# Kernel tuning notes

Measured on AMD Instinct MI355X. Metric: run time of the kernel, lower is better.

Reference implementation:

```python
import jax, jax.numpy as jnp
import numpy as np

B, T, C = 1, 4096, 1024
H = 16
D = C // H  # head_dim = 64


def setup_inputs() -> dict:
    key = jax.random.key(0)
    ks = jax.random.split(key, 9)
    s = 1.0 / np.sqrt(C)
    return {
        "x": jax.random.normal(ks[0], (B, T, C), dtype=jnp.float32),
        "Wq": jax.random.normal(ks[1], (C, C), dtype=jnp.float32) * s,
        "bq": jnp.zeros((C,), dtype=jnp.float32),
        "Wk": jax.random.normal(ks[2], (C, C), dtype=jnp.float32) * s,
        "bk": jnp.zeros((C,), dtype=jnp.float32),
        "Wv": jax.random.normal(ks[3], (C, C), dtype=jnp.float32) * s,
        "bv": jnp.zeros((C,), dtype=jnp.float32),
        "Wo": jax.random.normal(ks[4], (C, C), dtype=jnp.float32) * s,
        "bo": jnp.zeros((C,), dtype=jnp.float32),
    }


def reference(x, Wq, bq, Wk, bk, Wv, bv, Wo, bo):
    # QKV projections (torch Linear: y = x @ W.T + b)
    q = x @ Wq.T + bq
    k = x @ Wk.T + bk
    v = x @ Wv.T + bv
    # [B,T,C] -> [B,H,T,D]
    q = q.reshape(B, T, H, D).transpose(0, 2, 1, 3)
    k = k.reshape(B, T, H, D).transpose(0, 2, 1, 3)
    v = v.reshape(B, T, H, D).transpose(0, 2, 1, 3)
    scale = 1.0 / jnp.sqrt(jnp.asarray(D, dtype=q.dtype))
    scores = jnp.einsum("bhqd,bhkd->bhqk", q, k) * scale  # [B,H,T,T]
    attn = jax.nn.softmax(scores, axis=-1)
    out = jnp.einsum("bhqk,bhkd->bhqd", attn, v)  # [B,H,T,D]
    out = out.transpose(0, 2, 1, 3).reshape(B, T, C)
    return out @ Wo.T + bo
```

## Files before the change

### kernel.cpp

```cpp
#include <hip/hip_runtime.h>
#include <stdint.h>

#define T_SEQ 4096
#define CDIM  1024
#define NH    16
#define DH    64

typedef _Float16 half8 __attribute__((ext_vector_type(8)));
typedef _Float16 half4 __attribute__((ext_vector_type(4)));
typedef float    f32x4 __attribute__((ext_vector_type(4)));

#if __has_builtin(__builtin_amdgcn_exp2f)
#define EXP2F(x) __builtin_amdgcn_exp2f(x)
#else
#define EXP2F(x) exp2f(x)
#endif

#define MFMA_K32(a, b, c) __builtin_amdgcn_mfma_f32_16x16x32_f16(a, b, c, 0, 0, 0)
#define MFMA_K16(a, b, c) __builtin_amdgcn_mfma_f32_16x16x16f16(a, b, c, 0, 0, 0)

__device__ __forceinline__ void gl_lds16(const void* g, void* l) {
  __builtin_amdgcn_global_load_lds(
      (const __attribute__((address_space(1))) uint32_t*)g,
      (__attribute__((address_space(3))) uint32_t*)l, 16, 0, 0);
}

__global__ void cvt_kernel(const float* __restrict__ src, _Float16* __restrict__ dst, int n) {
  int i = (blockIdx.x * blockDim.x + threadIdx.x) * 8;
  if (i >= n) return;
  float4 f0 = *(const float4*)(src + i);
  float4 f1 = *(const float4*)(src + i + 4);
  half8 h = { (_Float16)f0.x, (_Float16)f0.y, (_Float16)f0.z, (_Float16)f0.w,
              (_Float16)f1.x, (_Float16)f1.y, (_Float16)f1.z, (_Float16)f1.w };
  *(half8*)(dst + i) = h;
}

__global__ void cvt_w4_kernel(const float* __restrict__ w0, const float* __restrict__ w1,
                              const float* __restrict__ w2, const float* __restrict__ w3,
                              _Float16* __restrict__ o0, _Float16* __restrict__ o1,
                              _Float16* __restrict__ o2, _Float16* __restrict__ o3) {
  const float* src = (blockIdx.y == 0) ? w0 : (blockIdx.y == 1) ? w1 : (blockIdx.y == 2) ? w2 : w3;
  _Float16*    dst = (blockIdx.y == 0) ? o0 : (blockIdx.y == 1) ? o1 : (blockIdx.y == 2) ? o2 : o3;
  int i = (blockIdx.x * blockDim.x + threadIdx.x) * 8;
  float4 f0 = *(const float4*)(src + i);
  float4 f1 = *(const float4*)(src + i + 4);
  half8 h = { (_Float16)f0.x, (_Float16)f0.y, (_Float16)f0.z, (_Float16)f0.w,
              (_Float16)f1.x, (_Float16)f1.y, (_Float16)f1.z, (_Float16)f1.w };
  *(half8*)(dst + i) = h;
}

__device__ __forceinline__ void gemm_core(const _Float16* __restrict__ A,
                                          const _Float16* __restrict__ Bm,
                                          _Float16* As, _Float16* Bs,
                                          int bm, int bn,
                                          f32x4 (&acc)[4][4]) {
  const int tid  = threadIdx.x;
  const int lane = tid & 63;
  const int wave = tid >> 6;
  const int waveM = wave >> 1, waveN = wave & 1;
  const int quad = lane >> 4, c16 = lane & 15;

  const int rs0 = wave * 32 + (lane >> 2);
  const int rs1 = rs0 + 16;
  const int dm0 = ((lane & 3) ^ ((rs0 >> 1) & 3)) * 8;
  const int dm1 = ((lane & 3) ^ ((rs1 >> 1) & 3)) * 8;

  const _Float16* gA0 = A  + (size_t)(bm * 128 + rs0) * CDIM + dm0;
  const _Float16* gA1 = A  + (size_t)(bm * 128 + rs1) * CDIM + dm1;
  const _Float16* gB0 = Bm + (size_t)(bn * 128 + rs0) * CDIM + dm0;
  const _Float16* gB1 = Bm + (size_t)(bn * 128 + rs1) * CDIM + dm1;
  _Float16* lA0 = As + wave * 1024;
  _Float16* lA1 = lA0 + 512;
  _Float16* lB0 = Bs + wave * 1024;
  _Float16* lB1 = lB0 + 512;

  const int xsw  = (c16 >> 1) & 3;
  const int offA = (waveM * 64 + c16) * 32 + ((quad ^ xsw) * 8);
  const int offB = (waveN * 64 + c16) * 32 + ((quad ^ xsw) * 8);

  for (int kk = 0; kk < 32; ++kk) {
    gl_lds16(gA0, lA0);
    gl_lds16(gA1, lA1);
    gl_lds16(gB0, lB0);
    gl_lds16(gB1, lB1);
    __syncthreads();
    half8 a[4], b[4];
#pragma unroll
    for (int i = 0; i < 4; ++i) a[i] = *(const half8*)(As + offA + i * 512);
#pragma unroll
    for (int i = 0; i < 4; ++i) b[i] = *(const half8*)(Bs + offB + i * 512);
#pragma unroll
    for (int mi = 0; mi < 4; ++mi)
#pragma unroll
      for (int ni = 0; ni < 4; ++ni)
        acc[mi][ni] = MFMA_K32(a[mi], b[ni], acc[mi][ni]);
    gA0 += 32; gA1 += 32; gB0 += 32; gB1 += 32;
    __syncthreads();
  }
}

__device__ __forceinline__ void gemm_core64(const _Float16* __restrict__ A,
                                            const _Float16* __restrict__ Bm,
                                            _Float16* As, _Float16* Bs,
                                            int bm, int bn,
                                            f32x4 (&acc)[2][4]) {
  const int tid  = threadIdx.x;
  const int lane = tid & 63;
  const int wave = tid >> 6;
  const int waveM = wave >> 1, waveN = wave & 1;
  const int quad = lane >> 4, c16 = lane & 15;

  const int rsA = wave * 16 + (lane >> 2);
  const int dmA = ((lane & 3) ^ ((rsA >> 1) & 3)) * 8;
  const int rs0 = wave * 32 + (lane >> 2);
  const int rs1 = rs0 + 16;
  const int dm0 = ((lane & 3) ^ ((rs0 >> 1) & 3)) * 8;
  const int dm1 = ((lane & 3) ^ ((rs1 >> 1) & 3)) * 8;

  const _Float16* gA0 = A  + (size_t)(bm * 64  + rsA) * CDIM + dmA;
  const _Float16* gB0 = Bm + (size_t)(bn * 128 + rs0) * CDIM + dm0;
  const _Float16* gB1 = Bm + (size_t)(bn * 128 + rs1) * CDIM + dm1;
  _Float16* lA0 = As + wave * 512;
  _Float16* lB0 = Bs + wave * 1024;
  _Float16* lB1 = lB0 + 512;

  const int xsw  = (c16 >> 1) & 3;
  const int offA = (waveM * 32 + c16) * 32 + ((quad ^ xsw) * 8);
  const int offB = (waveN * 64 + c16) * 32 + ((quad ^ xsw) * 8);

  for (int kk = 0; kk < 32; ++kk) {
    gl_lds16(gA0, lA0);
    gl_lds16(gB0, lB0);
    gl_lds16(gB1, lB1);
    __syncthreads();
    half8 a[2], b[4];
#pragma unroll
    for (int i = 0; i < 2; ++i) a[i] = *(const half8*)(As + offA + i * 512);
#pragma unroll
    for (int i = 0; i < 4; ++i) b[i] = *(const half8*)(Bs + offB + i * 512);
#pragma unroll
    for (int mi = 0; mi < 2; ++mi)
#pragma unroll
      for (int ni = 0; ni < 4; ++ni)
        acc[mi][ni] = MFMA_K32(a[mi], b[ni], acc[mi][ni]);
    gA0 += 32; gB0 += 32; gB1 += 32;
    __syncthreads();
  }
}

__global__ __launch_bounds__(256) void qkv_gemm(
    const _Float16* __restrict__ xh,
    const _Float16* __restrict__ wqh, const _Float16* __restrict__ wkh, const _Float16* __restrict__ wvh,
    const float* __restrict__ bq, const float* __restrict__ bk, const float* __restrict__ bv,
    _Float16* __restrict__ qh, _Float16* __restrict__ kh, _Float16* __restrict__ vth) {
  __shared__ __align__(16) _Float16 As[128 * 32];
  __shared__ __align__(16) _Float16 Bs[128 * 32];
  const int z = blockIdx.z;
  const _Float16* W   = (z == 0) ? wqh : ((z == 1) ? wkh : wvh);
  const float*    bias = (z == 0) ? bq  : ((z == 1) ? bk  : bv);

  f32x4 acc[4][4];
  const f32x4 zf = {0.f, 0.f, 0.f, 0.f};
#pragma unroll
  for (int i = 0; i < 4; ++i)
#pragma unroll
    for (int j = 0; j < 4; ++j) acc[i][j] = zf;

  gemm_core(xh, W, As, Bs, blockIdx.x, blockIdx.y, acc);

  const int lane = threadIdx.x & 63, wave = threadIdx.x >> 6;
  const int waveM = wave >> 1, waveN = wave & 1;
  const int quad = lane >> 4, c16 = lane & 15;
  const int rowb = blockIdx.x * 128 + waveM * 64;
  const int colb = blockIdx.y * 128 + waveN * 64;

  float bsv[4];
#pragma unroll
  for (int ni = 0; ni < 4; ++ni) bsv[ni] = bias[colb + ni * 16 + c16];

  if (z < 2) {
    _Float16* outp = (z == 0) ? qh : kh;
    const float scl = (z == 0) ? 0.18033688011112042f : 1.0f;
#pragma unroll
    for (int mi = 0; mi < 4; ++mi)
#pragma unroll
      for (int ni = 0; ni < 4; ++ni) {
        int col = colb + ni * 16 + c16;
        int hh = col >> 6, dd = col & 63;
#pragma unroll
        for (int r = 0; r < 4; ++r) {
          int row = rowb + mi * 16 + quad * 4 + r;
          outp[(size_t)(hh * T_SEQ + row) * DH + dd] = (_Float16)((acc[mi][ni][r] + bsv[ni]) * scl);
        }
      }
  } else {
#pragma unroll
    for (int mi = 0; mi < 4; ++mi)
#pragma unroll
      for (int ni = 0; ni < 4; ++ni) {
        int col  = colb + ni * 16 + c16;
        int row0 = rowb + mi * 16 + quad * 4;
        half4 h4;
#pragma unroll
        for (int r = 0; r < 4; ++r) h4[r] = (_Float16)(acc[mi][ni][r] + bsv[ni]);
        *(half4*)(vth + (size_t)col * T_SEQ + row0) = h4;
      }
  }
}

__global__ __launch_bounds__(256) void out_gemm(
    const _Float16* __restrict__ ctx, const _Float16* __restrict__ woh,
    const float* __restrict__ bo, float* __restrict__ out) {
  __shared__ __align__(16) _Float16 As[64 * 32];
  __shared__ __align__(16) _Float16 Bs[128 * 32];
  f32x4 acc[2][4];
  const f32x4 zf = {0.f, 0.f, 0.f, 0.f};
#pragma unroll
  for (int i = 0; i < 2; ++i)
#pragma unroll
    for (int j = 0; j < 4; ++j) acc[i][j] = zf;

  gemm_core64(ctx, woh, As, Bs, blockIdx.x, blockIdx.y, acc);

  const int lane = threadIdx.x & 63, wave = threadIdx.x >> 6;
  const int waveM = wave >> 1, waveN = wave & 1;
  const int quad = lane >> 4, c16 = lane & 15;
  const int rowb = blockIdx.x * 64 + waveM * 32;
  const int colb = blockIdx.y * 128 + waveN * 64;

  float bsv[4];
#pragma unroll
  for (int ni = 0; ni < 4; ++ni) bsv[ni] = bo[colb + ni * 16 + c16];

#pragma unroll
  for (int mi = 0; mi < 2; ++mi)
#pragma unroll
    for (int ni = 0; ni < 4; ++ni) {
      int col = colb + ni * 16 + c16;
#pragma unroll
      for (int r = 0; r < 4; ++r) {
        int row = rowb + mi * 16 + quad * 4 + r;
        out[(size_t)row * CDIM + col] = acc[mi][ni][r] + bsv[ni];
      }
    }
}

__global__ __launch_bounds__(256) void attn_kernel(
    const _Float16* __restrict__ qh, const _Float16* __restrict__ kh,
    const _Float16* __restrict__ vth, _Float16* __restrict__ ctx) {
  __shared__ __align__(16) _Float16 KV[2][2][64 * 64];

  const int tid = threadIdx.x, lane = tid & 63, wave = tid >> 6;
  const int quad = lane >> 4, c16 = lane & 15;
  const int h = blockIdx.y;
  const int qw = blockIdx.x * 128 + wave * 32;

  half8 qf[2][2];
#pragma unroll
  for (int qg = 0; qg < 2; ++qg)
#pragma unroll
    for (int c = 0; c < 2; ++c)
      qf[qg][c] = *(const half8*)(qh + (size_t)(h * T_SEQ + qw + qg * 16 + c16) * DH + c * 32 + quad * 8);

  const int rs0 = wave * 16 + (lane >> 3);
  const int rs1 = rs0 + 8;
  const int dm0 = ((lane & 7) ^ (rs0 & 7)) * 8;
  const int dm1 = ((lane & 7) ^ (rs1 & 7)) * 8;
  const _Float16* gK0 = kh  + (size_t)(h * T_SEQ + rs0) * DH + dm0;
  const _Float16* gK1 = kh  + (size_t)(h * T_SEQ + rs1) * DH + dm1;
  const _Float16* gV0 = vth + (size_t)(h * DH + rs0) * T_SEQ + dm0;
  const _Float16* gV1 = vth + (size_t)(h * DH + rs1) * T_SEQ + dm1;
  const int lo0 = wave * 1024, lo1 = wave * 1024 + 512;

  f32x4 o[2][4];
  f32x4 lacc[2];
  const f32x4 zf = {0.f, 0.f, 0.f, 0.f};
#pragma unroll
  for (int qg = 0; qg < 2; ++qg) {
#pragma unroll
    for (int db = 0; db < 4; ++db) o[qg][db] = zf;
    lacc[qg] = zf;
  }
  const half4 ones4 = { (_Float16)1, (_Float16)1, (_Float16)1, (_Float16)1 };

  gl_lds16(gK0, &KV[0][0][lo0]);
  gl_lds16(gK1, &KV[0][0][lo1]);
  gl_lds16(gV0, &KV[0][1][lo0]);
  gl_lds16(gV1, &KV[0][1][lo1]);
  gK0 += 64 * DH; gK1 += 64 * DH; gV0 += 64; gV1 += 64;
  __syncthreads();

  for (int kt = 0; kt < 64; ++kt) {
    const int b = kt & 1;
    if (kt < 63) {
      gl_lds16(gK0, &KV[b ^ 1][0][lo0]);
      gl_lds16(gK1, &KV[b ^ 1][0][lo1]);
      gl_lds16(gV0, &KV[b ^ 1][1][lo0]);
      gl_lds16(gV1, &KV[b ^ 1][1][lo1]);
      gK0 += 64 * DH; gK1 += 64 * DH; gV0 += 64; gV1 += 64;
    }
    const _Float16* Ks = &KV[b][0][0];
    const _Float16* Vs = &KV[b][1][0];

    const f32x4 minit = {-16.f, -16.f, -16.f, -16.f};
    f32x4 s[2][4];
#pragma unroll
    for (int qg = 0; qg < 2; ++qg)
#pragma unroll
      for (int kb = 0; kb < 4; ++kb) s[qg][kb] = minit;
#pragma unroll
    for (int c = 0; c < 2; ++c) {
#pragma unroll
      for (int kb = 0; kb < 4; ++kb) {
        int key = kb * 16 + c16;
        half8 ak = *(const half8*)(Ks + key * 64 + (((c * 4 + quad) ^ (key & 7)) * 8));
        s[0][kb] = MFMA_K32(ak, qf[0][c], s[0][kb]);
        s[1][kb] = MFMA_K32(ak, qf[1][c], s[1][kb]);
      }
    }

    half4 p[2][4];
#pragma unroll
    for (int qg = 0; qg < 2; ++qg)
#pragma unroll
      for (int kb = 0; kb < 4; ++kb)
#pragma unroll
        for (int r = 0; r < 4; ++r) p[qg][kb][r] = (_Float16)EXP2F(s[qg][kb][r]);

#pragma unroll
    for (int kb = 0; kb < 4; ++kb) {
      lacc[0] = MFMA_K16(ones4, p[0][kb], lacc[0]);
      lacc[1] = MFMA_K16(ones4, p[1][kb], lacc[1]);
    }

#pragma unroll
    for (int kb = 0; kb < 4; ++kb) {
      const int blk8 = kb * 2 + (quad >> 1);
      const int sub  = (quad & 1) * 4;
#pragma unroll
      for (int db = 0; db < 4; ++db) {
        int dd = db * 16 + c16;
        half4 av = *(const half4*)(Vs + dd * 64 + ((blk8 ^ (dd & 7)) * 8) + sub);
        o[0][db] = MFMA_K16(av, p[0][kb], o[0][db]);
        o[1][db] = MFMA_K16(av, p[1][kb], o[1][db]);
      }
    }

    __syncthreads();
  }

  _Float16* Pw = ((_Float16*)KV) + wave * (32 * 88);
#pragma unroll
  for (int qg = 0; qg < 2; ++qg) {
    float inv = 1.f / lacc[qg][0];
#pragma unroll
    for (int db = 0; db < 4; ++db) {
      half4 h4;
#pragma unroll
      for (int r = 0; r < 4; ++r) h4[r] = (_Float16)(o[qg][db][r] * inv);
      *(half4*)(Pw + (qg * 16 + c16) * 88 + db * 16 + quad * 4) = h4;
    }
  }
  const int q = lane >> 1, hv = lane & 1;
#pragma unroll
  for (int i = 0; i < 4; ++i) {
    half8 vv = *(const half8*)(Pw + q * 88 + hv * 32 + i * 8);
    *(half8*)(ctx + (size_t)(qw + q) * CDIM + h * DH + hv * 32 + i * 8) = vv;
  }
}

extern "C" void kernel_launch(void* const* d_in, const int* in_sizes, int n_in,
                              void* d_out, int out_size, void* d_ws, size_t ws_size,
                              hipStream_t stream) {
  const float* x  = (const float*)d_in[0];
  const float* Wq = (const float*)d_in[1];
  const float* bq = (const float*)d_in[2];
  const float* Wk = (const float*)d_in[3];
  const float* bk = (const float*)d_in[4];
  const float* Wv = (const float*)d_in[5];
  const float* bv = (const float*)d_in[6];
  const float* Wo = (const float*)d_in[7];
  const float* bo = (const float*)d_in[8];
  float* out = (float*)d_out;

  char* ws = (char*)d_ws;
  _Float16* xh  = (_Float16*)(ws);
  _Float16* qh  = (_Float16*)(ws + ((size_t)8  << 20));
  _Float16* kh  = (_Float16*)(ws + ((size_t)16 << 20));
  _Float16* vth = (_Float16*)(ws + ((size_t)24 << 20));
  _Float16* wqh = (_Float16*)(ws + ((size_t)32 << 20));
  _Float16* wkh = (_Float16*)(ws + ((size_t)34 << 20));
  _Float16* wvh = (_Float16*)(ws + ((size_t)36 << 20));
  _Float16* woh = (_Float16*)(ws + ((size_t)38 << 20));
  _Float16* ctx = xh;

  cvt_kernel<<<2048, 256, 0, stream>>>(x, xh, T_SEQ * CDIM);
  cvt_w4_kernel<<<dim3(512, 4), 256, 0, stream>>>(Wq, Wk, Wv, Wo, wqh, wkh, wvh, woh);

  qkv_gemm<<<dim3(32, 8, 3), 256, 0, stream>>>(xh, wqh, wkh, wvh, bq, bk, bv, qh, kh, vth);
  attn_kernel<<<dim3(32, 16), 256, 0, stream>>>(qh, kh, vth, ctx);
  out_gemm<<<dim3(64, 8), 256, 0, stream>>>(ctx, woh, bo, out);
}
```

Baseline: 241.9 us.

## Store V in MFMA fragment layout and load it directly to registers

The QKV GEMM now writes V in a pre-swizzled per-head, per-64-key-tile layout that matches the MFMA B-operand fragments. The attention kernel then loads V straight from global memory into registers with contiguous half4 loads, dropping the LDS staging for V and halving shared memory. The input and weight conversion kernels are merged into one launch. The trade-off is that the V loads now come from global/L2 each iteration with no async prefetch into LDS, which may expose latency and raises register use (16 extra half4 values).

```diff
diff --git a/kernel.cpp b/kernel.cpp
--- a/kernel.cpp
+++ b/kernel.cpp
@@ -25,22 +25,22 @@
       (__attribute__((address_space(3))) uint32_t*)l, 16, 0, 0);
 }
 
-__global__ void cvt_kernel(const float* __restrict__ src, _Float16* __restrict__ dst, int n) {
-  int i = (blockIdx.x * blockDim.x + threadIdx.x) * 8;
-  if (i >= n) return;
-  float4 f0 = *(const float4*)(src + i);
-  float4 f1 = *(const float4*)(src + i + 4);
-  half8 h = { (_Float16)f0.x, (_Float16)f0.y, (_Float16)f0.z, (_Float16)f0.w,
-              (_Float16)f1.x, (_Float16)f1.y, (_Float16)f1.z, (_Float16)f1.w };
-  *(half8*)(dst + i) = h;
-}
-
-__global__ void cvt_w4_kernel(const float* __restrict__ w0, const float* __restrict__ w1,
-                              const float* __restrict__ w2, const float* __restrict__ w3,
-                              _Float16* __restrict__ o0, _Float16* __restrict__ o1,
-                              _Float16* __restrict__ o2, _Float16* __restrict__ o3) {
-  const float* src = (blockIdx.y == 0) ? w0 : (blockIdx.y == 1) ? w1 : (blockIdx.y == 2) ? w2 : w3;
-  _Float16*    dst = (blockIdx.y == 0) ? o0 : (blockIdx.y == 1) ? o1 : (blockIdx.y == 2) ? o2 : o3;
+__global__ void cvt_all_kernel(const float* __restrict__ w0, const float* __restrict__ w1,
+                               const float* __restrict__ w2, const float* __restrict__ w3,
+                               const float* __restrict__ x,
+                               _Float16* __restrict__ o0, _Float16* __restrict__ o1,
+                               _Float16* __restrict__ o2, _Float16* __restrict__ o3,
+                               _Float16* __restrict__ xo) {
+  int y = blockIdx.y;
+  const float* src;
+  _Float16* dst;
+  if (y < 4) {
+    src = (y == 0) ? w0 : (y == 1) ? w1 : (y == 2) ? w2 : w3;
+    dst = (y == 0) ? o0 : (y == 1) ? o1 : (y == 2) ? o2 : o3;
+  } else {
+    src = x  + (size_t)(y - 4) * (CDIM * CDIM);
+    dst = xo + (size_t)(y - 4) * (CDIM * CDIM);
+  }
   int i = (blockIdx.x * blockDim.x + threadIdx.x) * 8;
   float4 f0 = *(const float4*)(src + i);
   float4 f1 = *(const float4*)(src + i + 4);
@@ -152,7 +152,7 @@
     const _Float16* __restrict__ xh,
     const _Float16* __restrict__ wqh, const _Float16* __restrict__ wkh, const _Float16* __restrict__ wvh,
     const float* __restrict__ bq, const float* __restrict__ bk, const float* __restrict__ bv,
-    _Float16* __restrict__ qh, _Float16* __restrict__ kh, _Float16* __restrict__ vth) {
+    _Float16* __restrict__ qh, _Float16* __restrict__ kh, _Float16* __restrict__ vfs) {
   __shared__ __align__(16) _Float16 As[128 * 32];
   __shared__ __align__(16) _Float16 Bs[128 * 32];
   const int z = blockIdx.z;
@@ -194,16 +194,19 @@
         }
       }
   } else {
+    const int kt = rowb >> 6;
 #pragma unroll
     for (int mi = 0; mi < 4; ++mi)
 #pragma unroll
       for (int ni = 0; ni < 4; ++ni) {
-        int col  = colb + ni * 16 + c16;
-        int row0 = rowb + mi * 16 + quad * 4;
+        int col = colb + ni * 16 + c16;
+        int hh = col >> 6, dd = col & 63;
+        int db = dd >> 4, cv = dd & 15;
         half4 h4;
 #pragma unroll
         for (int r = 0; r < 4; ++r) h4[r] = (_Float16)(acc[mi][ni][r] + bsv[ni]);
-        *(half4*)(vth + (size_t)col * T_SEQ + row0) = h4;
+        *(half4*)(vfs + (size_t)hh * (T_SEQ * 64) + (size_t)kt * 4096
+                      + (mi * 4 + db) * 256 + quad * 64 + cv * 4) = h4;
       }
   }
 }
@@ -247,8 +250,8 @@
 
 __global__ __launch_bounds__(256) void attn_kernel(
     const _Float16* __restrict__ qh, const _Float16* __restrict__ kh,
-    const _Float16* __restrict__ vth, _Float16* __restrict__ ctx) {
-  __shared__ __align__(16) _Float16 KV[2][2][64 * 64];
+    const _Float16* __restrict__ vfs, _Float16* __restrict__ ctx) {
+  __shared__ __align__(16) _Float16 Ks[2][64 * 64];
 
   const int tid = threadIdx.x, lane = tid & 63, wave = tid >> 6;
   const int quad = lane >> 4, c16 = lane & 15;
@@ -266,11 +269,11 @@
   const int rs1 = rs0 + 8;
   const int dm0 = ((lane & 7) ^ (rs0 & 7)) * 8;
   const int dm1 = ((lane & 7) ^ (rs1 & 7)) * 8;
-  const _Float16* gK0 = kh  + (size_t)(h * T_SEQ + rs0) * DH + dm0;
-  const _Float16* gK1 = kh  + (size_t)(h * T_SEQ + rs1) * DH + dm1;
-  const _Float16* gV0 = vth + (size_t)(h * DH + rs0) * T_SEQ + dm0;
-  const _Float16* gV1 = vth + (size_t)(h * DH + rs1) * T_SEQ + dm1;
+  const _Float16* gK0 = kh + (size_t)(h * T_SEQ + rs0) * DH + dm0;
+  const _Float16* gK1 = kh + (size_t)(h * T_SEQ + rs1) * DH + dm1;
   const int lo0 = wave * 1024, lo1 = wave * 1024 + 512;
+
+  const _Float16* vb = vfs + (size_t)h * (T_SEQ * 64) + lane * 4;
 
   f32x4 o[2][4];
   f32x4 lacc[2];
@@ -283,24 +286,27 @@
   }
   const half4 ones4 = { (_Float16)1, (_Float16)1, (_Float16)1, (_Float16)1 };
 
-  gl_lds16(gK0, &KV[0][0][lo0]);
-  gl_lds16(gK1, &KV[0][0][lo1]);
-  gl_lds16(gV0, &KV[0][1][lo0]);
-  gl_lds16(gV1, &KV[0][1][lo1]);
-  gK0 += 64 * DH; gK1 += 64 * DH; gV0 += 64; gV1 += 64;
+  gl_lds16(gK0, &Ks[0][lo0]);
+  gl_lds16(gK1, &Ks[0][lo1]);
+  gK0 += 64 * DH; gK1 += 64 * DH;
   __syncthreads();
 
   for (int kt = 0; kt < 64; ++kt) {
     const int b = kt & 1;
+
+    half4 av[16];
+    {
+      const _Float16* vp = vb + (size_t)kt * 4096;
+#pragma unroll
+      for (int f = 0; f < 16; ++f) av[f] = *(const half4*)(vp + f * 256);
+    }
+
     if (kt < 63) {
-      gl_lds16(gK0, &KV[b ^ 1][0][lo0]);
-      gl_lds16(gK1, &KV[b ^ 1][0][lo1]);
-      gl_lds16(gV0, &KV[b ^ 1][1][lo0]);
-      gl_lds16(gV1, &KV[b ^ 1][1][lo1]);
-      gK0 += 64 * DH; gK1 += 64 * DH; gV0 += 64; gV1 += 64;
-    }
-    const _Float16* Ks = &KV[b][0][0];
-    const _Float16* Vs = &KV[b][1][0];
+      gl_lds16(gK0, &Ks[b ^ 1][lo0]);
+      gl_lds16(gK1, &Ks[b ^ 1][lo1]);
+      gK0 += 64 * DH; gK1 += 64 * DH;
+    }
+    const _Float16* Kb = &Ks[b][0];
 
     const f32x4 minit = {-16.f, -16.f, -16.f, -16.f};
     f32x4 s[2][4];
@@ -313,7 +319,7 @@
 #pragma unroll
       for (int kb = 0; kb < 4; ++kb) {
         int key = kb * 16 + c16;
-        half8 ak = *(const half8*)(Ks + key * 64 + (((c * 4 + quad) ^ (key & 7)) * 8));
+        half8 ak = *(const half8*)(Kb + key * 64 + (((c * 4 + quad) ^ (key & 7)) * 8));
         s[0][kb] = MFMA_K32(ak, qf[0][c], s[0][kb]);
         s[1][kb] = MFMA_K32(ak, qf[1][c], s[1][kb]);
       }
@@ -334,22 +340,17 @@
     }
 
 #pragma unroll
-    for (int kb = 0; kb < 4; ++kb) {
-      const int blk8 = kb * 2 + (quad >> 1);
-      const int sub  = (quad & 1) * 4;
+    for (int kb = 0; kb < 4; ++kb)
 #pragma unroll
       for (int db = 0; db < 4; ++db) {
-        int dd = db * 16 + c16;
-        half4 av = *(const half4*)(Vs + dd * 64 + ((blk8 ^ (dd & 7)) * 8) + sub);
-        o[0][db] = MFMA_K16(av, p[0][kb], o[0][db]);
-        o[1][db] = MFMA_K16(av, p[1][kb], o[1][db]);
+        o[0][db] = MFMA_K16(av[kb * 4 + db], p[0][kb], o[0][db]);
+        o[1][db] = MFMA_K16(av[kb * 4 + db], p[1][kb], o[1][db]);
       }
-    }
 
     __syncthreads();
   }
 
-  _Float16* Pw = ((_Float16*)KV) + wave * (32 * 88);
+  _Float16* Pw = ((_Float16*)Ks) + wave * (32 * 64);
 #pragma unroll
   for (int qg = 0; qg < 2; ++qg) {
     float inv = 1.f / lacc[qg][0];
@@ -358,14 +359,18 @@
       half4 h4;
 #pragma unroll
       for (int r = 0; r < 4; ++r) h4[r] = (_Float16)(o[qg][db][r] * inv);
-      *(half4*)(Pw + (qg * 16 + c16) * 88 + db * 16 + quad * 4) = h4;
-    }
-  }
+      int row = qg * 16 + c16;
+      int g   = db * 2 + (quad >> 1);
+      *(half4*)(Pw + row * 64 + ((g ^ (row & 7)) * 8) + (quad & 1) * 4) = h4;
+    }
+  }
+  __syncthreads();
   const int q = lane >> 1, hv = lane & 1;
 #pragma unroll
   for (int i = 0; i < 4; ++i) {
-    half8 vv = *(const half8*)(Pw + q * 88 + hv * 32 + i * 8);
-    *(half8*)(ctx + (size_t)(qw + q) * CDIM + h * DH + hv * 32 + i * 8) = vv;
+    int g = hv * 4 + i;
+    half8 vv = *(const half8*)(Pw + q * 64 + ((g ^ (q & 7)) * 8));
+    *(half8*)(ctx + (size_t)(qw + q) * CDIM + h * DH + g * 8) = vv;
   }
 }
 
@@ -387,17 +392,16 @@
   _Float16* xh  = (_Float16*)(ws);
   _Float16* qh  = (_Float16*)(ws + ((size_t)8  << 20));
   _Float16* kh  = (_Float16*)(ws + ((size_t)16 << 20));
-  _Float16* vth = (_Float16*)(ws + ((size_t)24 << 20));
+  _Float16* vfs = (_Float16*)(ws + ((size_t)24 << 20));
   _Float16* wqh = (_Float16*)(ws + ((size_t)32 << 20));
   _Float16* wkh = (_Float16*)(ws + ((size_t)34 << 20));
   _Float16* wvh = (_Float16*)(ws + ((size_t)36 << 20));
   _Float16* woh = (_Float16*)(ws + ((size_t)38 << 20));
   _Float16* ctx = xh;
 
-  cvt_kernel<<<2048, 256, 0, stream>>>(x, xh, T_SEQ * CDIM);
-  cvt_w4_kernel<<<dim3(512, 4), 256, 0, stream>>>(Wq, Wk, Wv, Wo, wqh, wkh, wvh, woh);
-
-  qkv_gemm<<<dim3(32, 8, 3), 256, 0, stream>>>(xh, wqh, wkh, wvh, bq, bk, bv, qh, kh, vth);
-  attn_kernel<<<dim3(32, 16), 256, 0, stream>>>(qh, kh, vth, ctx);
+  cvt_all_kernel<<<dim3(512, 8), 256, 0, stream>>>(Wq, Wk, Wv, Wo, x,
+                                                   wqh, wkh, wvh, woh, xh);
+  qkv_gemm<<<dim3(32, 8, 3), 256, 0, stream>>>(xh, wqh, wkh, wvh, bq, bk, bv, qh, kh, vfs);
+  attn_kernel<<<dim3(32, 16), 256, 0, stream>>>(qh, kh, vfs, ctx);
   out_gemm<<<dim3(64, 8), 256, 0, stream>>>(ctx, woh, bo, out);
 }
```

After: 257.1 us. 6.3% more time.
